# Optimization experiments

Hardware: AMD Instinct MI355X
Metric: run time of the kernel (lower is better)

Reference implementation:

```python
import jax, jax.numpy as jnp
import numpy as np

HIDDEN = 4096
N_HEADS = 32
N_KV_HEADS = 8
HEAD_DIM = 128
ROPE_THETA = 1e6
RMS_EPS = 1e-6
SEQ = 2048


def setup_inputs() -> dict:
    key = jax.random.key(0)
    k1, k2, k3 = jax.random.split(key, 3)
    hidden_states = jax.random.normal(k1, (SEQ, HIDDEN), dtype=jnp.float32)
    # fused QKV weight: [hidden, (H + 2*Hkv) * head_dim]
    qkv_out = (N_HEADS + 2 * N_KV_HEADS) * HEAD_DIM
    w_qkv = jax.random.normal(k2, (HIDDEN, qkv_out), dtype=jnp.float32) * (HIDDEN ** -0.5)
    w_o = jax.random.normal(k3, (N_HEADS * HEAD_DIM, HIDDEN), dtype=jnp.float32) * ((N_HEADS * HEAD_DIM) ** -0.5)
    q_norm_w = jnp.ones((HEAD_DIM,), dtype=jnp.float32)
    k_norm_w = jnp.ones((HEAD_DIM,), dtype=jnp.float32)
    # NeoX-style rotary tables [T, head_dim/2]
    pos = jnp.arange(SEQ, dtype=jnp.float32)
    inv_freq = 1.0 / (ROPE_THETA ** (jnp.arange(0, HEAD_DIM, 2, dtype=jnp.float32) / HEAD_DIM))
    freqs = pos[:, None] * inv_freq[None, :]  # [T, d/2]
    cos = jnp.cos(freqs)
    sin = jnp.sin(freqs)
    return {"hidden_states": hidden_states, "cos": cos, "sin": sin,
            "w_qkv": w_qkv, "w_o": w_o, "q_norm_w": q_norm_w, "k_norm_w": k_norm_w}


def _rms_norm(x, w, eps=RMS_EPS):
    # per-head RMSNorm over last dim (head_dim)
    var = jnp.mean(jnp.square(x), axis=-1, keepdims=True)
    return x * jax.lax.rsqrt(var + eps) * w


def _rope(x, cos, sin):
    # NeoX rotate-half: x split into two halves of head_dim
    d2 = x.shape[-1] // 2
    x1, x2 = x[..., :d2], x[..., d2:]
    c = cos[:, None, :]  # [T,1,d/2] broadcast over heads
    s = sin[:, None, :]
    return jnp.concatenate([x1 * c - x2 * s, x2 * c + x1 * s], axis=-1)


def reference(hidden_states, cos, sin, w_qkv, w_o, q_norm_w, k_norm_w):
    T = hidden_states.shape[0]
    H, Hkv, D = N_HEADS, N_KV_HEADS, HEAD_DIM
    G = H // Hkv  # GQA group size
    scale = D ** -0.5

    qkv = hidden_states @ w_qkv  # [T, (H+2Hkv)*D]
    q, k, v = jnp.split(qkv, [H * D, (H + Hkv) * D], axis=1)
    q = q.reshape(T, H, D)
    k = k.reshape(T, Hkv, D)
    v = v.reshape(T, Hkv, D)

    q = _rms_norm(q, q_norm_w)
    k = _rms_norm(k, k_norm_w)
    q = _rope(q, cos, sin)
    k = _rope(k, cos, sin)

    # GQA: group query heads onto shared KV heads
    qg = q.reshape(T, Hkv, G, D)
    scores = jnp.einsum('qhgd,khd->hgqk', qg, k) * scale  # [Hkv,G,T,T]
    causal = jnp.tril(jnp.ones((T, T), dtype=bool))
    scores = jnp.where(causal, scores, jnp.float32(-1e30))
    probs = jax.nn.softmax(scores, axis=-1)
    out = jnp.einsum('hgqk,khd->qhgd', probs, v).reshape(T, H * D)
    return out @ w_o  # [T, hidden]
```

## Files before the change

kernel.cpp:

```cpp
#include <hip/hip_runtime.h>
#include <stdint.h>

#define SEQ   2048
#define HID   4096
#define NQH   32
#define NKVH  8
#define HD    128
#define QKVN  6144

typedef uint16_t u16;
typedef __attribute__((ext_vector_type(8))) short bf16x8;
typedef __attribute__((ext_vector_type(4))) float f32x4;
typedef __attribute__((ext_vector_type(4))) unsigned int u32x4;

static __device__ __forceinline__ float bf2f(u16 h){
  union { float f; unsigned int u; } v; v.u = ((unsigned int)h) << 16; return v.f;
}
static __device__ __forceinline__ u16 f2bf(float f){
  unsigned int u = __float_as_uint(f);
  return (u16)((u + 0x7fffu + ((u >> 16) & 1u)) >> 16);
}
static __device__ __forceinline__ f32x4 mfma16(bf16x8 a, bf16x8 b, f32x4 c){
  return __builtin_amdgcn_mfma_f32_16x16x32_bf16(a, b, c, 0, 0, 0);
}
static __device__ __forceinline__ void gload16(const void* g, void* l){
  __builtin_amdgcn_global_load_lds((const __attribute__((address_space(1))) void*)g,
                                   (__attribute__((address_space(3))) void*)l, 16, 0, 0);
}

__global__ void k_cvt(const float* __restrict__ src, u16* __restrict__ dst, int n4){
  int i = blockIdx.x * blockDim.x + threadIdx.x;
  if (i >= n4) return;
  float4 v = ((const float4*)src)[i];
  uint2 o;
  o.x = (unsigned)f2bf(v.x) | ((unsigned)f2bf(v.y) << 16);
  o.y = (unsigned)f2bf(v.z) | ((unsigned)f2bf(v.w) << 16);
  ((uint2*)dst)[i] = o;
}

__global__ void k_addf(const float* __restrict__ a, float* __restrict__ o, int n4){
  int i = blockIdx.x * blockDim.x + threadIdx.x;
  if (i >= n4) return;
  float4 x = ((const float4*)o)[i];
  float4 y = ((const float4*)a)[i];
  x.x += y.x; x.y += y.y; x.z += y.z; x.w += y.w;
  ((float4*)o)[i] = x;
}

__global__ void k_transpose_cvt(const float* __restrict__ src, u16* __restrict__ dst, int K, int N){
  __shared__ float t[32][33];
  int n0 = blockIdx.x * 32, k0 = blockIdx.y * 32;
  int tx = threadIdx.x, ty = threadIdx.y;
#pragma unroll
  for (int i = 0; i < 32; i += 8)
    t[ty + i][tx] = src[(size_t)(k0 + ty + i) * N + n0 + tx];
  __syncthreads();
#pragma unroll
  for (int i = 0; i < 32; i += 8)
    dst[(size_t)(n0 + ty + i) * K + k0 + tx] = f2bf(t[tx][ty + i]);
}

template<int OUTBF, int SPLITK, int XBC, int NBY>
__global__ __launch_bounds__(512) void k_gemm(const u16* __restrict__ A, const u16* __restrict__ Bt,
                                              void* __restrict__ Cv0, void* __restrict__ Cv1,
                                              int M, int N, int K){
  __shared__ __align__(16) u16 Asm[2][2][128][64];
  __shared__ __align__(16) u16 Bsm[2][2][128][64];
  const int tid = threadIdx.x, lane = tid & 63, wid = tid >> 6;
  const int wm = wid >> 2, wn = wid & 3;
  const int l16 = lane & 15, lhi = lane >> 4;
  const int rx = l16 & 7;
  const int bid = blockIdx.x;
  const int xcd = bid & 7, jj = bid >> 3;
  const int bcol_i = xcd * XBC + jj % XBC;
  const int rest = jj / XBC;
  const int brow_i = rest % NBY;
  const int kz = (SPLITK > 1) ? (rest / NBY) : 0;
  const size_t brow = (size_t)brow_i * 256, bcol = (size_t)bcol_i * 256;
  const int kbeg = kz * (K / SPLITK);
  void* Cv = (kz == 0) ? Cv0 : Cv1;

  const f32x4 vz = {0.f, 0.f, 0.f, 0.f};
  f32x4 acc[8][4];
#pragma unroll
  for (int m = 0; m < 8; m++)
#pragma unroll
    for (int n = 0; n < 4; n++) acc[m][n] = vz;

  const int srow = lane >> 3;
  const int sg   = (lane & 7) ^ srow;
  const u16* Ags = A  + (brow + wid*8 + srow) * (size_t)K + sg*8 + kbeg;
  const u16* Bgs = Bt + (bcol + wid*8 + srow) * (size_t)K + sg*8 + kbeg;
  const int NT = (K / SPLITK) >> 6;
  const int NU = NT >> 1;

#define FRA(buf, mi, kh) (*(const bf16x8*)&Asm[buf][wm][(mi)*16 + l16][(((kh)*4 + lhi) ^ rx) << 3])
#define FRB(buf, ni, kh) (*(const bf16x8*)&Bsm[buf][wn >> 1][(wn & 1)*64 + (ni)*16 + l16][(((kh)*4 + lhi) ^ rx) << 3])
#define STG_A(tile, half) do{ if ((tile) < NT){                                  \
    const size_t ko_ = (size_t)((half)*128) * K + (size_t)(tile) * 64;           \
    gload16(Ags + ko_,                &Asm[(tile)&1][half][wid*8][0]);           \
    gload16(Ags + ko_ + (size_t)64*K, &Asm[(tile)&1][half][64 + wid*8][0]); } }while(0)
#define STG_B(tile, half) do{ if ((tile) < NT){                                  \
    const size_t ko_ = (size_t)((half)*128) * K + (size_t)(tile) * 64;           \
    gload16(Bgs + ko_,                &Bsm[(tile)&1][half][wid*8][0]);           \
    gload16(Bgs + ko_ + (size_t)64*K, &Bsm[(tile)&1][half][64 + wid*8][0]); } }while(0)

  STG_B(0, 0); STG_B(0, 1); STG_A(0, 0); STG_A(0, 1); STG_B(1, 0); STG_B(1, 1);
  asm volatile("s_waitcnt vmcnt(4)" ::: "memory");
  __builtin_amdgcn_sched_barrier(0);
  __builtin_amdgcn_s_barrier();

  bf16x8 fA[4][2], fB01[2][2], fB23[2][2];
  for (int u = 0; u < NU; ++u){
    const int t = 2 * u;
#pragma unroll
    for (int mi = 0; mi < 4; ++mi){ fA[mi][0] = FRA(0, mi, 0); fA[mi][1] = FRA(0, mi, 1); }
#pragma unroll
    for (int ni = 0; ni < 2; ++ni){ fB01[ni][0] = FRB(0, ni, 0); fB01[ni][1] = FRB(0, ni, 1); }
    STG_A(t + 1, 0);
    asm volatile("s_waitcnt lgkmcnt(8)" ::: "memory");
    __builtin_amdgcn_s_barrier();
    asm volatile("s_waitcnt lgkmcnt(0)" ::: "memory");
    __builtin_amdgcn_sched_barrier(0);
    __builtin_amdgcn_s_setprio(1);
#pragma unroll
    for (int kh = 0; kh < 2; ++kh)
#pragma unroll
      for (int mi = 0; mi < 4; ++mi)
#pragma unroll
        for (int ni = 0; ni < 2; ++ni)
          acc[mi][ni] = mfma16(fA[mi][kh], fB01[ni][kh], acc[mi][ni]);
    __builtin_amdgcn_s_setprio(0);
    __builtin_amdgcn_s_barrier();
#pragma unroll
    for (int ni = 0; ni < 2; ++ni){ fB23[ni][0] = FRB(0, 2 + ni, 0); fB23[ni][1] = FRB(0, 2 + ni, 1); }
    STG_A(t + 1, 1);
    __builtin_amdgcn_s_barrier();
    asm volatile("s_waitcnt lgkmcnt(0)" ::: "memory");
    __builtin_amdgcn_sched_barrier(0);
    __builtin_amdgcn_s_setprio(1);
#pragma unroll
    for (int kh = 0; kh < 2; ++kh)
#pragma unroll
      for (int mi = 0; mi < 4; ++mi)
#pragma unroll
        for (int ni = 0; ni < 2; ++ni)
          acc[mi][2 + ni] = mfma16(fA[mi][kh], fB23[ni][kh], acc[mi][2 + ni]);
    __builtin_amdgcn_s_setprio(0);
    __builtin_amdgcn_s_barrier();
#pragma unroll
    for (int mi = 0; mi < 4; ++mi){ fA[mi][0] = FRA(0, 4 + mi, 0); fA[mi][1] = FRA(0, 4 + mi, 1); }
    STG_B(t + 2, 0);
    __builtin_amdgcn_s_barrier();
    asm volatile("s_waitcnt lgkmcnt(0)" ::: "memory");
    __builtin_amdgcn_sched_barrier(0);
    __builtin_amdgcn_s_setprio(1);
#pragma unroll
    for (int kh = 0; kh < 2; ++kh)
#pragma unroll
      for (int mi = 0; mi < 4; ++mi)
#pragma unroll
        for (int ni = 0; ni < 2; ++ni)
          acc[4 + mi][ni] = mfma16(fA[mi][kh], fB01[ni][kh], acc[4 + mi][ni]);
    __builtin_amdgcn_s_setprio(0);
    __builtin_amdgcn_s_barrier();
    STG_B(t + 2, 1);
    __builtin_amdgcn_s_barrier();
    asm volatile("s_waitcnt lgkmcnt(0)" ::: "memory");
    __builtin_amdgcn_sched_barrier(0);
    __builtin_amdgcn_s_setprio(1);
#pragma unroll
    for (int kh = 0; kh < 2; ++kh)
#pragma unroll
      for (int mi = 0; mi < 4; ++mi)
#pragma unroll
        for (int ni = 0; ni < 2; ++ni)
          acc[4 + mi][2 + ni] = mfma16(fA[mi][kh], fB23[ni][kh], acc[4 + mi][2 + ni]);
    __builtin_amdgcn_s_setprio(0);
    if (u == NU - 1) asm volatile("s_waitcnt vmcnt(0)" ::: "memory");
    else             asm volatile("s_waitcnt vmcnt(4)" ::: "memory");
    __builtin_amdgcn_sched_barrier(0);
    __builtin_amdgcn_s_barrier();
#pragma unroll
    for (int mi = 0; mi < 4; ++mi){ fA[mi][0] = FRA(1, mi, 0); fA[mi][1] = FRA(1, mi, 1); }
#pragma unroll
    for (int ni = 0; ni < 2; ++ni){ fB01[ni][0] = FRB(1, ni, 0); fB01[ni][1] = FRB(1, ni, 1); }
    STG_A(t + 2, 0);
    asm volatile("s_waitcnt lgkmcnt(8)" ::: "memory");
    __builtin_amdgcn_s_barrier();
    asm volatile("s_waitcnt lgkmcnt(0)" ::: "memory");
    __builtin_amdgcn_sched_barrier(0);
    __builtin_amdgcn_s_setprio(1);
#pragma unroll
    for (int kh = 0; kh < 2; ++kh)
#pragma unroll
      for (int mi = 0; mi < 4; ++mi)
#pragma unroll
        for (int ni = 0; ni < 2; ++ni)
          acc[mi][ni] = mfma16(fA[mi][kh], fB01[ni][kh], acc[mi][ni]);
    __builtin_amdgcn_s_setprio(0);
    __builtin_amdgcn_s_barrier();
#pragma unroll
    for (int ni = 0; ni < 2; ++ni){ fB23[ni][0] = FRB(1, 2 + ni, 0); fB23[ni][1] = FRB(1, 2 + ni, 1); }
    STG_A(t + 2, 1);
    __builtin_amdgcn_s_barrier();
    asm volatile("s_waitcnt lgkmcnt(0)" ::: "memory");
    __builtin_amdgcn_sched_barrier(0);
    __builtin_amdgcn_s_setprio(1);
#pragma unroll
    for (int kh = 0; kh < 2; ++kh)
#pragma unroll
      for (int mi = 0; mi < 4; ++mi)
#pragma unroll
        for (int ni = 0; ni < 2; ++ni)
          acc[mi][2 + ni] = mfma16(fA[mi][kh], fB23[ni][kh], acc[mi][2 + ni]);
    __builtin_amdgcn_s_setprio(0);
    __builtin_amdgcn_s_barrier();
#pragma unroll
    for (int mi = 0; mi < 4; ++mi){ fA[mi][0] = FRA(1, 4 + mi, 0); fA[mi][1] = FRA(1, 4 + mi, 1); }
    STG_B(t + 3, 0);
    __builtin_amdgcn_s_barrier();
    asm volatile("s_waitcnt lgkmcnt(0)" ::: "memory");
    __builtin_amdgcn_sched_barrier(0);
    __builtin_amdgcn_s_setprio(1);
#pragma unroll
    for (int kh = 0; kh < 2; ++kh)
#pragma unroll
      for (int mi = 0; mi < 4; ++mi)
#pragma unroll
        for (int ni = 0; ni < 2; ++ni)
          acc[4 + mi][ni] = mfma16(fA[mi][kh], fB01[ni][kh], acc[4 + mi][ni]);
    __builtin_amdgcn_s_setprio(0);
    __builtin_amdgcn_s_barrier();
    STG_B(t + 3, 1);
    __builtin_amdgcn_s_barrier();
    asm volatile("s_waitcnt lgkmcnt(0)" ::: "memory");
    __builtin_amdgcn_sched_barrier(0);
    __builtin_amdgcn_s_setprio(1);
#pragma unroll
    for (int kh = 0; kh < 2; ++kh)
#pragma unroll
      for (int mi = 0; mi < 4; ++mi)
#pragma unroll
        for (int ni = 0; ni < 2; ++ni)
          acc[4 + mi][2 + ni] = mfma16(fA[mi][kh], fB23[ni][kh], acc[4 + mi][2 + ni]);
    __builtin_amdgcn_s_setprio(0);
    asm volatile("s_waitcnt vmcnt(4)" ::: "memory");
    __builtin_amdgcn_sched_barrier(0);
    __builtin_amdgcn_s_barrier();
  }
#undef FRA
#undef FRB
#undef STG_A
#undef STG_B

#pragma unroll
  for (int mi = 0; mi < 8; mi++)
#pragma unroll
    for (int ni = 0; ni < 4; ni++)
#pragma unroll
      for (int i = 0; i < 4; i++){
        size_t row = brow + wm*128 + mi*16 + lhi*4 + i;
        size_t col = bcol + wn*64 + ni*16 + l16;
        if (OUTBF) ((u16*)Cv)[row * (size_t)N + col] = f2bf(acc[mi][ni][i]);
        else       ((float*)Cv)[row * (size_t)N + col] = acc[mi][ni][i];
      }
}

__global__ __launch_bounds__(256) void k_rmsrope(const u16* __restrict__ qkv, const float* __restrict__ cosp,
                                                 const float* __restrict__ sinp, const float* __restrict__ qw,
                                                 const float* __restrict__ kw, u16* __restrict__ Qr,
                                                 u16* __restrict__ Kr){
  int t = blockIdx.x;
  int lane = threadIdx.x & 63, w = threadIdx.x >> 6;
  int hh = blockIdx.y * 4 + w;
  bool isq = hh < NQH;
  int hl = isq ? hh : hh - NQH;
  const u16* src = qkv + (size_t)t * QKVN + (isq ? hl * HD : NQH * HD + hl * HD);
  unsigned u = *(const unsigned*)(src + 2 * lane);
  float x0 = bf2f((u16)(u & 0xffffu)), x1 = bf2f((u16)(u >> 16));
  float ss = x0 * x0 + x1 * x1;
#pragma unroll
  for (int m = 1; m < 64; m <<= 1) ss += __shfl_xor(ss, m);
  float rs = rsqrtf(ss * (1.f / HD) + 1e-6f);
  const float* wp = isq ? qw : kw;
  float w0 = wp[2 * lane], w1 = wp[2 * lane + 1];
  float xn0 = x0 * rs * w0, xn1 = x1 * rs * w1;
  float p0 = __shfl_xor(xn0, 32), p1 = __shfl_xor(xn1, 32);
  int j0 = (2 * lane) & 63;
  float c0 = cosp[t * 64 + j0], c1 = cosp[t * 64 + j0 + 1];
  float s0 = sinp[t * 64 + j0], s1 = sinp[t * 64 + j0 + 1];
  float o0, o1;
  if (lane < 32){ o0 = xn0 * c0 - p0 * s0; o1 = xn1 * c1 - p1 * s1; }
  else          { o0 = xn0 * c0 + p0 * s0; o1 = xn1 * c1 + p1 * s1; }
  if (isq){ o0 *= 0.08838834764831845f; o1 *= 0.08838834764831845f; }
  u16* dst = isq ? (Qr + ((size_t)hl * SEQ + t) * HD) : (Kr + ((size_t)hl * SEQ + t) * HD);
  *(unsigned*)(dst + 2 * lane) = (unsigned)f2bf(o0) | ((unsigned)f2bf(o1) << 16);
}

__global__ void k_vt(const u16* __restrict__ qkv, u16* __restrict__ VT){
  __shared__ u16 t[32][33];
  int t0 = blockIdx.x * 32, d0 = blockIdx.y * 32, hv = blockIdx.z;
  int tx = threadIdx.x, ty = threadIdx.y;
#pragma unroll
  for (int i = 0; i < 32; i += 8)
    t[ty + i][tx] = qkv[(size_t)(t0 + ty + i) * QKVN + (NQH + NKVH) * HD + hv * HD + d0 + tx];
  __syncthreads();
#pragma unroll
  for (int i = 0; i < 32; i += 8)
    VT[((size_t)hv * HD + d0 + ty + i) * SEQ + t0 + tx] = t[tx][ty + i];
}

__global__ __launch_bounds__(512) void k_attn(const u16* __restrict__ Q, const u16* __restrict__ Kg,
                                              const u16* __restrict__ VTg, u16* __restrict__ AO){
  __shared__ __align__(16) u16 Ksm[2][128][128];
  __shared__ __align__(16) u16 Vsm[128][128];
  __shared__ __align__(16) u16 Psm[8][16][136];
  int tid = threadIdx.x, lane = tid & 63, wid = tid >> 6;
  int l16 = lane & 15, lhi = lane >> 4;
  int bid = blockIdx.x;
  int kvg = bid & 7, rr = bid >> 3;
  int J = 15 - (rr >> 2);
  int hq = kvg * 4 + (rr & 3);
  int qb = J * 128;
  const u16* Kh = Kg  + (size_t)kvg * SEQ * HD;
  const u16* Vh = VTg + (size_t)kvg * HD * SEQ;
  const u16* Qh = Q   + (size_t)hq * SEQ * HD;

  bf16x8 qf[4];
#pragma unroll
  for (int ks = 0; ks < 4; ks++)
    qf[ks] = *(const bf16x8*)(Qh + (size_t)(qb + wid*16 + l16) * HD + ks*32 + lhi*8);

  const f32x4 vz = {0.f, 0.f, 0.f, 0.f};
  f32x4 o[8];
  float mrow[4], lrow[4];
#pragma unroll
  for (int n = 0; n < 8; n++) o[n] = vz;
#pragma unroll
  for (int i = 0; i < 4; i++){ mrow[i] = -1e30f; lrow[i] = 0.f; }

  int rsub = lane >> 4, g = lane & 15;
  const u16 *Ks0, *Ks1, *Ks2, *Ks3, *Vs0, *Vs1, *Vs2, *Vs3;
  {
    int r0 = wid*16 + 0*4 + rsub, r1 = wid*16 + 1*4 + rsub;
    int r2 = wid*16 + 2*4 + rsub, r3 = wid*16 + 3*4 + rsub;
    Ks0 = Kh + (size_t)r0 * HD + ((g ^ (r0 & 7)) << 3);
    Ks1 = Kh + (size_t)r1 * HD + ((g ^ (r1 & 7)) << 3);
    Ks2 = Kh + (size_t)r2 * HD + ((g ^ (r2 & 7)) << 3);
    Ks3 = Kh + (size_t)r3 * HD + ((g ^ (r3 & 7)) << 3);
    Vs0 = Vh + (size_t)r0 * SEQ + ((g ^ (r0 & 7)) << 3);
    Vs1 = Vh + (size_t)r1 * SEQ + ((g ^ (r1 & 7)) << 3);
    Vs2 = Vh + (size_t)r2 * SEQ + ((g ^ (r2 & 7)) << 3);
    Vs3 = Vh + (size_t)r3 * SEQ + ((g ^ (r3 & 7)) << 3);
  }

  gload16(Ks0, &Ksm[0][wid*16 +  0][0]);
  gload16(Ks1, &Ksm[0][wid*16 +  4][0]);
  gload16(Ks2, &Ksm[0][wid*16 +  8][0]);
  gload16(Ks3, &Ksm[0][wid*16 + 12][0]);
  asm volatile("s_waitcnt vmcnt(0)" ::: "memory");
  __builtin_amdgcn_sched_barrier(0);
  __builtin_amdgcn_s_barrier();

  int ntr = J + 1;
  int wrow0 = qb + wid*16;
  for (int t = 0; t < ntr; t++){
    int cur = t & 1, nxt = cur ^ 1;
    int kt0 = t << 7;
    bool pf = (t + 1 < ntr);
    gload16(Vs0 + kt0, &Vsm[wid*16 +  0][0]);
    gload16(Vs1 + kt0, &Vsm[wid*16 +  4][0]);
    gload16(Vs2 + kt0, &Vsm[wid*16 +  8][0]);
    gload16(Vs3 + kt0, &Vsm[wid*16 + 12][0]);
    if (pf){
      size_t ko = (size_t)(kt0 + 128) * HD;
      gload16(Ks0 + ko, &Ksm[nxt][wid*16 +  0][0]);
      gload16(Ks1 + ko, &Ksm[nxt][wid*16 +  4][0]);
      gload16(Ks2 + ko, &Ksm[nxt][wid*16 +  8][0]);
      gload16(Ks3 + ko, &Ksm[nxt][wid*16 + 12][0]);
    }
    f32x4 s[8];
#pragma unroll
    for (int n = 0; n < 8; n++) s[n] = vz;
    const u16* kbase = &Ksm[cur][0][0];
    __builtin_amdgcn_s_setprio(1);
#pragma unroll
    for (int n = 0; n < 8; n++){
      int row = n*16 + l16, rxk = row & 7;
#pragma unroll
      for (int ks = 0; ks < 4; ks++){
        bf16x8 kf = *(const bf16x8*)(kbase + row*128 + (((ks*4 + lhi) ^ rxk) << 3));
        s[n] = mfma16(qf[ks], kf, s[n]);
      }
    }
    __builtin_amdgcn_s_setprio(0);
    if (kt0 + 127 > wrow0){
#pragma unroll
      for (int n = 0; n < 8; n++)
#pragma unroll
        for (int i = 0; i < 4; i++)
          if (kt0 + n*16 + l16 > wrow0 + lhi*4 + i) s[n][i] = -1e30f;
    }
#pragma unroll
    for (int i = 0; i < 4; i++){
      float tm = fmaxf(fmaxf(fmaxf(s[0][i], s[1][i]), fmaxf(s[2][i], s[3][i])),
                       fmaxf(fmaxf(s[4][i], s[5][i]), fmaxf(s[6][i], s[7][i])));
      tm = fmaxf(tm, __shfl_xor(tm, 1));
      tm = fmaxf(tm, __shfl_xor(tm, 2));
      tm = fmaxf(tm, __shfl_xor(tm, 4));
      tm = fmaxf(tm, __shfl_xor(tm, 8));
      float nm = fmaxf(mrow[i], tm);
      float sc = __expf(mrow[i] - nm);
      mrow[i] = nm;
      float rsum = 0.f;
#pragma unroll
      for (int n = 0; n < 8; n++){
        float p = __expf(s[n][i] - nm);
        s[n][i] = p;
        rsum += p;
      }
      rsum += __shfl_xor(rsum, 1);
      rsum += __shfl_xor(rsum, 2);
      rsum += __shfl_xor(rsum, 4);
      rsum += __shfl_xor(rsum, 8);
      lrow[i] = lrow[i] * sc + rsum;
#pragma unroll
      for (int n = 0; n < 8; n++) o[n][i] *= sc;
    }
#pragma unroll
    for (int n = 0; n < 8; n++)
#pragma unroll
      for (int i = 0; i < 4; i++)
        Psm[wid][lhi*4 + i][n*16 + l16] = f2bf(s[n][i]);
    if (pf) asm volatile("s_waitcnt vmcnt(4)" ::: "memory");
    else    asm volatile("s_waitcnt vmcnt(0)" ::: "memory");
    __builtin_amdgcn_sched_barrier(0);
    __builtin_amdgcn_s_barrier();
    __builtin_amdgcn_sched_barrier(0);
    __builtin_amdgcn_s_setprio(1);
#pragma unroll
    for (int ksv = 0; ksv < 4; ksv++){
      bf16x8 pa = *(const bf16x8*)&Psm[wid][l16][ksv*32 + lhi*8];
#pragma unroll
      for (int n = 0; n < 8; n++){
        int row = n*16 + l16;
        bf16x8 vb = *(const bf16x8*)(&Vsm[0][0] + row*128 + (((ksv*4 + lhi) ^ (row & 7)) << 3));
        o[n] = mfma16(pa, vb, o[n]);
      }
    }
    __builtin_amdgcn_s_setprio(0);
    asm volatile("s_waitcnt vmcnt(0)" ::: "memory");
    __builtin_amdgcn_sched_barrier(0);
    __builtin_amdgcn_s_barrier();
  }
  float inv[4];
#pragma unroll
  for (int i = 0; i < 4; i++) inv[i] = 1.f / lrow[i];
#pragma unroll
  for (int n = 0; n < 8; n++)
#pragma unroll
    for (int i = 0; i < 4; i++){
      int trow = wrow0 + lhi*4 + i;
      AO[(size_t)trow * HID + hq * HD + n*16 + l16] = f2bf(o[n][i] * inv[i]);
    }
}

extern "C" void kernel_launch(void* const* d_in, const int* in_sizes, int n_in,
                              void* d_out, int out_size, void* d_ws, size_t ws_size,
                              hipStream_t stream){
  const float* hs   = (const float*)d_in[0];
  const float* cosp = (const float*)d_in[1];
  const float* sinp = (const float*)d_in[2];
  const float* wqkv = (const float*)d_in[3];
  const float* wo   = (const float*)d_in[4];
  const float* qw   = (const float*)d_in[5];
  const float* kw   = (const float*)d_in[6];
  float* out = (float*)d_out;
  char* ws = (char*)d_ws;
  u16* XB    = (u16*)(ws + 0);
  u16* WQKVT = (u16*)(ws + 16777216);
  u16* WOT   = (u16*)(ws + 0);
  float* SCR = (float*)(ws + 33554432);
  u16* QKV   = (u16*)(ws + 67108864);
  u16* QR    = (u16*)(ws + 92274688);
  u16* KR    = (u16*)(ws + 109051904);
  u16* VTB   = (u16*)(ws + 113246208);
  u16* AOB   = (u16*)(ws + 117440512);

  k_cvt<<<(SEQ * HID / 4 + 255) / 256, 256, 0, stream>>>(hs, XB, SEQ * HID / 4);
  k_transpose_cvt<<<dim3(QKVN / 32, HID / 32), dim3(32, 8), 0, stream>>>(wqkv, WQKVT, HID, QKVN);
  k_gemm<1, 1, 3, 8><<<192, 512, 0, stream>>>(XB, WQKVT, QKV, nullptr, SEQ, QKVN, HID);
  k_transpose_cvt<<<dim3(HID / 32, HID / 32), dim3(32, 8), 0, stream>>>(wo, WOT, HID, HID);
  k_rmsrope<<<dim3(SEQ, 10), 256, 0, stream>>>(QKV, cosp, sinp, qw, kw, QR, KR);
  k_vt<<<dim3(SEQ / 32, HD / 32, NKVH), dim3(32, 8), 0, stream>>>(QKV, VTB);
  k_attn<<<512, 512, 0, stream>>>(QR, KR, VTB, AOB);
  k_gemm<0, 2, 2, 8><<<256, 512, 0, stream>>>(AOB, WOT, out, SCR, SEQ, HID, HID);
  k_addf<<<SEQ * HID / 4 / 256, 256, 0, stream>>>(SCR, out, SEQ * HID / 4);
}
```

Measured before the change: 344.9 us.

## Add 256x192-tile QKV GEMM and process 256 query rows per attention block

Replaces the QKV projection GEMM with a new kernel using 256x192 output tiles over 256 workgroups, software-pipelined with interleaved LDS fragment reads and global staging. The attention kernel now handles 256 query rows per block, with each wave owning 32 rows, so each K/V tile loaded into LDS is reused by twice as many queries. It also skips fully masked causal tiles per wave. The aim is fewer waves, better use of all CUs for the GEMM, and less K/V traffic. The cost is higher register pressure, half as many attention blocks, and more causal load imbalance.

```diff
diff --git a/kernel.cpp b/kernel.cpp
--- a/kernel.cpp
+++ b/kernel.cpp
@@ -58,6 +58,195 @@
 #pragma unroll
   for (int i = 0; i < 32; i += 8)
     dst[(size_t)(n0 + ty + i) * K + k0 + tx] = f2bf(t[tx][ty + i]);
+}
+
+__global__ __launch_bounds__(512) void k_gemm192(const u16* __restrict__ A, const u16* __restrict__ Bt,
+                                                 u16* __restrict__ Cv, int M, int N, int K){
+  __shared__ __align__(16) u16 Asm[2][256][64];
+  __shared__ __align__(16) u16 Bsm[2][192][64];
+  const int tid = threadIdx.x, lane = tid & 63, wid = tid >> 6;
+  const int wm = wid >> 2, wn = wid & 3;
+  const int l16 = lane & 15, lhi = lane >> 4;
+  const int rx = l16 & 7;
+  const int bid = blockIdx.x;
+  const int xcd = bid & 7, jj = bid >> 3;
+  const size_t bcol = (size_t)(xcd * 4 + jj % 4) * 192;
+  const size_t brow = (size_t)((jj / 4) & 7) * 256;
+
+  const f32x4 vz = {0.f, 0.f, 0.f, 0.f};
+  f32x4 acc[8][3];
+#pragma unroll
+  for (int m = 0; m < 8; m++)
+#pragma unroll
+    for (int n = 0; n < 3; n++) acc[m][n] = vz;
+
+  const int srow = lane >> 3;
+  const int sg   = (lane & 7) ^ srow;
+  const u16* Ags = A  + (brow + wid*8 + srow) * (size_t)K + sg*8;
+  const u16* Bgs = Bt + (bcol + wid*8 + srow) * (size_t)K + sg*8;
+  const int NT = K >> 6, NU = NT >> 1;
+
+#define FRA(buf, mi, kh) (*(const bf16x8*)&Asm[buf][wm*128 + (mi)*16 + l16][(((kh)*4 + lhi) ^ rx) << 3])
+#define FRB(buf, ni, kh) (*(const bf16x8*)&Bsm[buf][wn*48 + (ni)*16 + l16][(((kh)*4 + lhi) ^ rx) << 3])
+#define STG_A(tile, half) do{ if ((tile) < NT){                                  \
+    const size_t ko_ = (size_t)((half)*128) * K + (size_t)(tile) * 64;           \
+    gload16(Ags + ko_,                &Asm[(tile)&1][(half)*128 + wid*8][0]);     \
+    gload16(Ags + ko_ + (size_t)64*K, &Asm[(tile)&1][(half)*128 + 64 + wid*8][0]); } }while(0)
+#define STG_B(tile, r) do{ if ((tile) < NT){                                     \
+    const size_t ko_ = (size_t)((r)*64) * K + (size_t)(tile) * 64;               \
+    gload16(Bgs + ko_, &Bsm[(tile)&1][(r)*64 + wid*8][0]); } }while(0)
+
+  STG_B(0,0); STG_B(0,1); STG_B(0,2);
+  STG_A(0,0); STG_A(0,1);
+  STG_B(1,0); STG_B(1,1); STG_B(1,2);
+  asm volatile("s_waitcnt vmcnt(3)" ::: "memory");
+  __builtin_amdgcn_sched_barrier(0);
+  __builtin_amdgcn_s_barrier();
+
+  bf16x8 fA[4][2], fB01[2][2], fB2[2];
+  for (int u = 0; u < NU; ++u){
+    const int t = 2 * u;
+#pragma unroll
+    for (int mi = 0; mi < 4; ++mi){ fA[mi][0] = FRA(0, mi, 0); fA[mi][1] = FRA(0, mi, 1); }
+#pragma unroll
+    for (int ni = 0; ni < 2; ++ni){ fB01[ni][0] = FRB(0, ni, 0); fB01[ni][1] = FRB(0, ni, 1); }
+    STG_A(t + 1, 0);
+    asm volatile("s_waitcnt lgkmcnt(8)" ::: "memory");
+    __builtin_amdgcn_s_barrier();
+    asm volatile("s_waitcnt lgkmcnt(0)" ::: "memory");
+    __builtin_amdgcn_sched_barrier(0);
+    __builtin_amdgcn_s_setprio(1);
+#pragma unroll
+    for (int kh = 0; kh < 2; ++kh)
+#pragma unroll
+      for (int mi = 0; mi < 4; ++mi)
+#pragma unroll
+        for (int ni = 0; ni < 2; ++ni)
+          acc[mi][ni] = mfma16(fA[mi][kh], fB01[ni][kh], acc[mi][ni]);
+    __builtin_amdgcn_s_setprio(0);
+    __builtin_amdgcn_s_barrier();
+    fB2[0] = FRB(0, 2, 0); fB2[1] = FRB(0, 2, 1);
+    STG_A(t + 1, 1);
+    __builtin_amdgcn_s_barrier();
+    asm volatile("s_waitcnt lgkmcnt(0)" ::: "memory");
+    __builtin_amdgcn_sched_barrier(0);
+    __builtin_amdgcn_s_setprio(1);
+#pragma unroll
+    for (int kh = 0; kh < 2; ++kh)
+#pragma unroll
+      for (int mi = 0; mi < 4; ++mi)
+        acc[mi][2] = mfma16(fA[mi][kh], fB2[kh], acc[mi][2]);
+    __builtin_amdgcn_s_setprio(0);
+    __builtin_amdgcn_s_barrier();
+#pragma unroll
+    for (int mi = 0; mi < 4; ++mi){ fA[mi][0] = FRA(0, 4 + mi, 0); fA[mi][1] = FRA(0, 4 + mi, 1); }
+    STG_B(t + 2, 0);
+    __builtin_amdgcn_s_barrier();
+    asm volatile("s_waitcnt lgkmcnt(0)" ::: "memory");
+    __builtin_amdgcn_sched_barrier(0);
+    __builtin_amdgcn_s_setprio(1);
+#pragma unroll
+    for (int kh = 0; kh < 2; ++kh)
+#pragma unroll
+      for (int mi = 0; mi < 4; ++mi)
+#pragma unroll
+        for (int ni = 0; ni < 2; ++ni)
+          acc[4 + mi][ni] = mfma16(fA[mi][kh], fB01[ni][kh], acc[4 + mi][ni]);
+    __builtin_amdgcn_s_setprio(0);
+    __builtin_amdgcn_s_barrier();
+    STG_B(t + 2, 1); STG_B(t + 2, 2);
+    __builtin_amdgcn_s_barrier();
+    asm volatile("s_waitcnt lgkmcnt(0)" ::: "memory");
+    __builtin_amdgcn_sched_barrier(0);
+    __builtin_amdgcn_s_setprio(1);
+#pragma unroll
+    for (int kh = 0; kh < 2; ++kh)
+#pragma unroll
+      for (int mi = 0; mi < 4; ++mi)
+        acc[4 + mi][2] = mfma16(fA[mi][kh], fB2[kh], acc[4 + mi][2]);
+    __builtin_amdgcn_s_setprio(0);
+    if (u == NU - 1) asm volatile("s_waitcnt vmcnt(0)" ::: "memory");
+    else             asm volatile("s_waitcnt vmcnt(3)" ::: "memory");
+    __builtin_amdgcn_sched_barrier(0);
+    __builtin_amdgcn_s_barrier();
+#pragma unroll
+    for (int mi = 0; mi < 4; ++mi){ fA[mi][0] = FRA(1, mi, 0); fA[mi][1] = FRA(1, mi, 1); }
+#pragma unroll
+    for (int ni = 0; ni < 2; ++ni){ fB01[ni][0] = FRB(1, ni, 0); fB01[ni][1] = FRB(1, ni, 1); }
+    STG_A(t + 2, 0);
+    asm volatile("s_waitcnt lgkmcnt(8)" ::: "memory");
+    __builtin_amdgcn_s_barrier();
+    asm volatile("s_waitcnt lgkmcnt(0)" ::: "memory");
+    __builtin_amdgcn_sched_barrier(0);
+    __builtin_amdgcn_s_setprio(1);
+#pragma unroll
+    for (int kh = 0; kh < 2; ++kh)
+#pragma unroll
+      for (int mi = 0; mi < 4; ++mi)
+#pragma unroll
+        for (int ni = 0; ni < 2; ++ni)
+          acc[mi][ni] = mfma16(fA[mi][kh], fB01[ni][kh], acc[mi][ni]);
+    __builtin_amdgcn_s_setprio(0);
+    __builtin_amdgcn_s_barrier();
+    fB2[0] = FRB(1, 2, 0); fB2[1] = FRB(1, 2, 1);
+    STG_A(t + 2, 1);
+    __builtin_amdgcn_s_barrier();
+    asm volatile("s_waitcnt lgkmcnt(0)" ::: "memory");
+    __builtin_amdgcn_sched_barrier(0);
+    __builtin_amdgcn_s_setprio(1);
+#pragma unroll
+    for (int kh = 0; kh < 2; ++kh)
+#pragma unroll
+      for (int mi = 0; mi < 4; ++mi)
+        acc[mi][2] = mfma16(fA[mi][kh], fB2[kh], acc[mi][2]);
+    __builtin_amdgcn_s_setprio(0);
+    __builtin_amdgcn_s_barrier();
+#pragma unroll
+    for (int mi = 0; mi < 4; ++mi){ fA[mi][0] = FRA(1, 4 + mi, 0); fA[mi][1] = FRA(1, 4 + mi, 1); }
+    STG_B(t + 3, 0);
+    __builtin_amdgcn_s_barrier();
+    asm volatile("s_waitcnt lgkmcnt(0)" ::: "memory");
+    __builtin_amdgcn_sched_barrier(0);
+    __builtin_amdgcn_s_setprio(1);
+#pragma unroll
+    for (int kh = 0; kh < 2; ++kh)
+#pragma unroll
+      for (int mi = 0; mi < 4; ++mi)
+#pragma unroll
+        for (int ni = 0; ni < 2; ++ni)
+          acc[4 + mi][ni] = mfma16(fA[mi][kh], fB01[ni][kh], acc[4 + mi][ni]);
+    __builtin_amdgcn_s_setprio(0);
+    __builtin_amdgcn_s_barrier();
+    STG_B(t + 3, 1); STG_B(t + 3, 2);
+    __builtin_amdgcn_s_barrier();
+    asm volatile("s_waitcnt lgkmcnt(0)" ::: "memory");
+    __builtin_amdgcn_sched_barrier(0);
+    __builtin_amdgcn_s_setprio(1);
+#pragma unroll
+    for (int kh = 0; kh < 2; ++kh)
+#pragma unroll
+      for (int mi = 0; mi < 4; ++mi)
+        acc[4 + mi][2] = mfma16(fA[mi][kh], fB2[kh], acc[4 + mi][2]);
+    __builtin_amdgcn_s_setprio(0);
+    asm volatile("s_waitcnt vmcnt(3)" ::: "memory");
+    __builtin_amdgcn_sched_barrier(0);
+    __builtin_amdgcn_s_barrier();
+  }
+#undef FRA
+#undef FRB
+#undef STG_A
+#undef STG_B
+
+#pragma unroll
+  for (int mi = 0; mi < 8; mi++)
+#pragma unroll
+    for (int ni = 0; ni < 3; ni++)
+#pragma unroll
+      for (int i = 0; i < 4; i++){
+        size_t row = brow + wm*128 + mi*16 + lhi*4 + i;
+        size_t col = bcol + wn*48 + ni*16 + l16;
+        Cv[row * (size_t)N + col] = f2bf(acc[mi][ni][i]);
+      }
 }
 
 template<int OUTBF, int SPLITK, int XBC, int NBY>
@@ -320,25 +509,30 @@
   int l16 = lane & 15, lhi = lane >> 4;
   int bid = blockIdx.x;
   int kvg = bid & 7, rr = bid >> 3;
-  int J = 15 - (rr >> 2);
+  int J = 7 - (rr >> 2);
   int hq = kvg * 4 + (rr & 3);
-  int qb = J * 128;
+  int qb = J * 256;
   const u16* Kh = Kg  + (size_t)kvg * SEQ * HD;
   const u16* Vh = VTg + (size_t)kvg * HD * SEQ;
   const u16* Qh = Q   + (size_t)hq * SEQ * HD;
 
-  bf16x8 qf[4];
-#pragma unroll
-  for (int ks = 0; ks < 4; ks++)
-    qf[ks] = *(const bf16x8*)(Qh + (size_t)(qb + wid*16 + l16) * HD + ks*32 + lhi*8);
+  bf16x8 qf[2][4];
+#pragma unroll
+  for (int m = 0; m < 2; m++)
+#pragma unroll
+    for (int ks = 0; ks < 4; ks++)
+      qf[m][ks] = *(const bf16x8*)(Qh + (size_t)(qb + wid*32 + m*16 + l16) * HD + ks*32 + lhi*8);
 
   const f32x4 vz = {0.f, 0.f, 0.f, 0.f};
-  f32x4 o[8];
-  float mrow[4], lrow[4];
-#pragma unroll
-  for (int n = 0; n < 8; n++) o[n] = vz;
-#pragma unroll
-  for (int i = 0; i < 4; i++){ mrow[i] = -1e30f; lrow[i] = 0.f; }
+  f32x4 o[2][8];
+  float mrow[2][4], lrow[2][4];
+#pragma unroll
+  for (int m = 0; m < 2; m++){
+#pragma unroll
+    for (int n = 0; n < 8; n++) o[m][n] = vz;
+#pragma unroll
+    for (int i = 0; i < 4; i++){ mrow[m][i] = -1e30f; lrow[m][i] = 0.f; }
+  }
 
   int rsub = lane >> 4, g = lane & 15;
   const u16 *Ks0, *Ks1, *Ks2, *Ks3, *Vs0, *Vs1, *Vs2, *Vs3;
@@ -363,8 +557,8 @@
   __builtin_amdgcn_sched_barrier(0);
   __builtin_amdgcn_s_barrier();
 
-  int ntr = J + 1;
-  int wrow0 = qb + wid*16;
+  int ntr = 2*J + 2;
+  int wbase = qb + wid*32;
   for (int t = 0; t < ntr; t++){
     int cur = t & 1, nxt = cur ^ 1;
     int kt0 = t << 7;
@@ -380,90 +574,118 @@
       gload16(Ks2 + ko, &Ksm[nxt][wid*16 +  8][0]);
       gload16(Ks3 + ko, &Ksm[nxt][wid*16 + 12][0]);
     }
-    f32x4 s[8];
-#pragma unroll
-    for (int n = 0; n < 8; n++) s[n] = vz;
-    const u16* kbase = &Ksm[cur][0][0];
-    __builtin_amdgcn_s_setprio(1);
-#pragma unroll
-    for (int n = 0; n < 8; n++){
-      int row = n*16 + l16, rxk = row & 7;
-#pragma unroll
-      for (int ks = 0; ks < 4; ks++){
-        bf16x8 kf = *(const bf16x8*)(kbase + row*128 + (((ks*4 + lhi) ^ rxk) << 3));
-        s[n] = mfma16(qf[ks], kf, s[n]);
+    bool act = (kt0 <= wbase + 31);
+    f32x4 s[2][8];
+    if (act){
+#pragma unroll
+      for (int m = 0; m < 2; m++)
+#pragma unroll
+        for (int n = 0; n < 8; n++) s[m][n] = vz;
+      const u16* kbase = &Ksm[cur][0][0];
+      __builtin_amdgcn_s_setprio(1);
+#pragma unroll
+      for (int n = 0; n < 8; n++){
+        int row = n*16 + l16, rxk = row & 7;
+#pragma unroll
+        for (int ks = 0; ks < 4; ks++){
+          bf16x8 kf = *(const bf16x8*)(kbase + row*128 + (((ks*4 + lhi) ^ rxk) << 3));
+          s[0][n] = mfma16(qf[0][ks], kf, s[0][n]);
+          s[1][n] = mfma16(qf[1][ks], kf, s[1][n]);
+        }
       }
+      __builtin_amdgcn_s_setprio(0);
+      if (kt0 + 127 > wbase){
+#pragma unroll
+        for (int m = 0; m < 2; m++)
+#pragma unroll
+          for (int n = 0; n < 8; n++)
+#pragma unroll
+            for (int i = 0; i < 4; i++)
+              if (kt0 + n*16 + l16 > wbase + m*16 + lhi*4 + i) s[m][n][i] = -1e30f;
+      }
+#pragma unroll
+      for (int m = 0; m < 2; m++)
+#pragma unroll
+        for (int i = 0; i < 4; i++){
+          float tm = fmaxf(fmaxf(fmaxf(s[m][0][i], s[m][1][i]), fmaxf(s[m][2][i], s[m][3][i])),
+                           fmaxf(fmaxf(s[m][4][i], s[m][5][i]), fmaxf(s[m][6][i], s[m][7][i])));
+          tm = fmaxf(tm, __shfl_xor(tm, 1));
+          tm = fmaxf(tm, __shfl_xor(tm, 2));
+          tm = fmaxf(tm, __shfl_xor(tm, 4));
+          tm = fmaxf(tm, __shfl_xor(tm, 8));
+          float nm = fmaxf(mrow[m][i], tm);
+          float sc = __expf(mrow[m][i] - nm);
+          mrow[m][i] = nm;
+          float rsum = 0.f;
+#pragma unroll
+          for (int n = 0; n < 8; n++){
+            float p = __expf(s[m][n][i] - nm);
+            s[m][n][i] = p;
+            rsum += p;
+          }
+          rsum += __shfl_xor(rsum, 1);
+          rsum += __shfl_xor(rsum, 2);
+          rsum += __shfl_xor(rsum, 4);
+          rsum += __shfl_xor(rsum, 8);
+          lrow[m][i] = lrow[m][i] * sc + rsum;
+#pragma unroll
+          for (int n = 0; n < 8; n++) o[m][n][i] *= sc;
+        }
     }
-    __builtin_amdgcn_s_setprio(0);
-    if (kt0 + 127 > wrow0){
-#pragma unroll
-      for (int n = 0; n < 8; n++)
-#pragma unroll
-        for (int i = 0; i < 4; i++)
-          if (kt0 + n*16 + l16 > wrow0 + lhi*4 + i) s[n][i] = -1e30f;
-    }
-#pragma unroll
-    for (int i = 0; i < 4; i++){
-      float tm = fmaxf(fmaxf(fmaxf(s[0][i], s[1][i]), fmaxf(s[2][i], s[3][i])),
-                       fmaxf(fmaxf(s[4][i], s[5][i]), fmaxf(s[6][i], s[7][i])));
-      tm = fmaxf(tm, __shfl_xor(tm, 1));
-      tm = fmaxf(tm, __shfl_xor(tm, 2));
-      tm = fmaxf(tm, __shfl_xor(tm, 4));
-      tm = fmaxf(tm, __shfl_xor(tm, 8));
-      float nm = fmaxf(mrow[i], tm);
-      float sc = __expf(mrow[i] - nm);
-      mrow[i] = nm;
-      float rsum = 0.f;
-#pragma unroll
-      for (int n = 0; n < 8; n++){
-        float p = __expf(s[n][i] - nm);
-        s[n][i] = p;
-        rsum += p;
-      }
-      rsum += __shfl_xor(rsum, 1);
-      rsum += __shfl_xor(rsum, 2);
-      rsum += __shfl_xor(rsum, 4);
-      rsum += __shfl_xor(rsum, 8);
-      lrow[i] = lrow[i] * sc + rsum;
-#pragma unroll
-      for (int n = 0; n < 8; n++) o[n][i] *= sc;
-    }
-#pragma unroll
-    for (int n = 0; n < 8; n++)
-#pragma unroll
-      for (int i = 0; i < 4; i++)
-        Psm[wid][lhi*4 + i][n*16 + l16] = f2bf(s[n][i]);
     if (pf) asm volatile("s_waitcnt vmcnt(4)" ::: "memory");
     else    asm volatile("s_waitcnt vmcnt(0)" ::: "memory");
     __builtin_amdgcn_sched_barrier(0);
     __builtin_amdgcn_s_barrier();
     __builtin_amdgcn_sched_barrier(0);
-    __builtin_amdgcn_s_setprio(1);
-#pragma unroll
-    for (int ksv = 0; ksv < 4; ksv++){
-      bf16x8 pa = *(const bf16x8*)&Psm[wid][l16][ksv*32 + lhi*8];
-#pragma unroll
-      for (int n = 0; n < 8; n++){
-        int row = n*16 + l16;
-        bf16x8 vb = *(const bf16x8*)(&Vsm[0][0] + row*128 + (((ksv*4 + lhi) ^ (row & 7)) << 3));
-        o[n] = mfma16(pa, vb, o[n]);
+    if (act){
+      bf16x8 pa0[4], pa1[4];
+#pragma unroll
+      for (int n = 0; n < 8; n++)
+#pragma unroll
+        for (int i = 0; i < 4; i++)
+          Psm[wid][lhi*4 + i][n*16 + l16] = f2bf(s[0][n][i]);
+#pragma unroll
+      for (int ksv = 0; ksv < 4; ksv++)
+        pa0[ksv] = *(const bf16x8*)&Psm[wid][l16][ksv*32 + lhi*8];
+      __builtin_amdgcn_sched_barrier(0);
+#pragma unroll
+      for (int n = 0; n < 8; n++)
+#pragma unroll
+        for (int i = 0; i < 4; i++)
+          Psm[wid][lhi*4 + i][n*16 + l16] = f2bf(s[1][n][i]);
+#pragma unroll
+      for (int ksv = 0; ksv < 4; ksv++)
+        pa1[ksv] = *(const bf16x8*)&Psm[wid][l16][ksv*32 + lhi*8];
+      __builtin_amdgcn_s_setprio(1);
+#pragma unroll
+      for (int ksv = 0; ksv < 4; ksv++){
+#pragma unroll
+        for (int n = 0; n < 8; n++){
+          int row = n*16 + l16;
+          bf16x8 vb = *(const bf16x8*)(&Vsm[0][0] + row*128 + (((ksv*4 + lhi) ^ (row & 7)) << 3));
+          o[0][n] = mfma16(pa0[ksv], vb, o[0][n]);
+          o[1][n] = mfma16(pa1[ksv], vb, o[1][n]);
+        }
       }
+      __builtin_amdgcn_s_setprio(0);
     }
-    __builtin_amdgcn_s_setprio(0);
     asm volatile("s_waitcnt vmcnt(0)" ::: "memory");
     __builtin_amdgcn_sched_barrier(0);
     __builtin_amdgcn_s_barrier();
   }
-  float inv[4];
-#pragma unroll
-  for (int i = 0; i < 4; i++) inv[i] = 1.f / lrow[i];
-#pragma unroll
-  for (int n = 0; n < 8; n++)
-#pragma unroll
-    for (int i = 0; i < 4; i++){
-      int trow = wrow0 + lhi*4 + i;
-      AO[(size_t)trow * HID + hq * HD + n*16 + l16] = f2bf(o[n][i] * inv[i]);
-    }
+#pragma unroll
+  for (int m = 0; m < 2; m++){
+    float inv[4];
+#pragma unroll
+    for (int i = 0; i < 4; i++) inv[i] = 1.f / lrow[m][i];
+#pragma unroll
+    for (int n = 0; n < 8; n++)
+#pragma unroll
+      for (int i = 0; i < 4; i++){
+        int trow = wbase + m*16 + lhi*4 + i;
+        AO[(size_t)trow * HID + hq * HD + n*16 + l16] = f2bf(o[m][n][i] * inv[i]);
+      }
+  }
 }
 
 extern "C" void kernel_launch(void* const* d_in, const int* in_sizes, int n_in,
@@ -490,11 +712,11 @@
 
   k_cvt<<<(SEQ * HID / 4 + 255) / 256, 256, 0, stream>>>(hs, XB, SEQ * HID / 4);
   k_transpose_cvt<<<dim3(QKVN / 32, HID / 32), dim3(32, 8), 0, stream>>>(wqkv, WQKVT, HID, QKVN);
-  k_gemm<1, 1, 3, 8><<<192, 512, 0, stream>>>(XB, WQKVT, QKV, nullptr, SEQ, QKVN, HID);
+  k_gemm192<<<256, 512, 0, stream>>>(XB, WQKVT, QKV, SEQ, QKVN, HID);
   k_transpose_cvt<<<dim3(HID / 32, HID / 32), dim3(32, 8), 0, stream>>>(wo, WOT, HID, HID);
   k_rmsrope<<<dim3(SEQ, 10), 256, 0, stream>>>(QKV, cosp, sinp, qw, kw, QR, KR);
   k_vt<<<dim3(SEQ / 32, HD / 32, NKVH), dim3(32, 8), 0, stream>>>(QKV, VTB);
-  k_attn<<<512, 512, 0, stream>>>(QR, KR, VTB, AOB);
+  k_attn<<<256, 512, 0, stream>>>(QR, KR, VTB, AOB);
   k_gemm<0, 2, 2, 8><<<256, 512, 0, stream>>>(AOB, WOT, out, SCR, SEQ, HID, HID);
   k_addf<<<SEQ * HID / 4 / 256, 256, 0, stream>>>(SCR, out, SEQ * HID / 4);
 }
```

After: 374.9 us. 1.09x slower.
